# Kernel tuning notes

Measured on AMD Instinct MI355X. Metric: run time of the kernel, lower is better.

The kernel has to match this reference:

```python
import jax, jax.numpy as jnp
import numpy as np
from jax import lax

B, T, C = 32, 4096, 64
K, D, H, OUT = 256, 64, 512, 6

def _conv1d(x, w, b, stride):
    # x: [B, Cin, L], w: [Cout, Cin, k]
    y = lax.conv_general_dilated(x, w, (stride,), 'SAME',
                                 dimension_numbers=('NCH', 'OIH', 'NCH'))
    return y + b[None, :, None]

def _lstm_layer(x, wih, whh, b):
    # x: [B, T, in]; wih: [4H, in]; whh: [4H, H]
    Bb = x.shape[0]
    Hh = whh.shape[1]
    xg = jnp.einsum('bti,gi->btg', x, wih) + b          # [B, T, 4H] precomputed input gates
    def step(carry, g_t):
        h, c = carry
        gates = g_t + h @ whh.T
        i, f, g, o = jnp.split(gates, 4, axis=-1)        # torch gate order i,f,g,o
        i = jax.nn.sigmoid(i); f = jax.nn.sigmoid(f)
        g = jnp.tanh(g);       o = jax.nn.sigmoid(o)
        c = f * c + i * g
        h = o * jnp.tanh(c)
        return (h, c), h
    init = (jnp.zeros((Bb, Hh), x.dtype), jnp.zeros((Bb, Hh), x.dtype))
    _, hs = lax.scan(step, init, jnp.swapaxes(xg, 0, 1))
    return jnp.swapaxes(hs, 0, 1)                        # [B, T, H]

def setup_inputs() -> dict:
    key = jax.random.key(0)
    ks = jax.random.split(key, 12)
    s = 0.02
    return {
        'x':       jax.random.normal(ks[0], (B, T, C), jnp.float32),
        'conv_w1': jax.random.normal(ks[1], (64, 1, 4), jnp.float32) * s,
        'conv_b1': jnp.zeros((64,), jnp.float32),
        'conv_w2': jax.random.normal(ks[2], (64, 64, 4), jnp.float32) * s,
        'conv_b2': jnp.zeros((64,), jnp.float32),
        'conv_w3': jax.random.normal(ks[3], (64, 64, 3), jnp.float32) * s,
        'conv_b3': jnp.zeros((64,), jnp.float32),
        'codebook': jax.random.normal(ks[4], (K, D), jnp.float32),
        'wih0': jax.random.normal(ks[5], (4 * H, D), jnp.float32) * s,
        'whh0': jax.random.normal(ks[6], (4 * H, H), jnp.float32) * s,
        'bl0':  jnp.zeros((4 * H,), jnp.float32),
        'wih1': jax.random.normal(ks[7], (4 * H, H), jnp.float32) * s,
        'whh1': jax.random.normal(ks[8], (4 * H, H), jnp.float32) * s,
        'bl1':  jnp.zeros((4 * H,), jnp.float32),
        'w_out': jax.random.normal(ks[9], (OUT, H), jnp.float32) * s,
        'b_out': jnp.zeros((OUT,), jnp.float32),
    }

def reference(x, conv_w1, conv_b1, conv_w2, conv_b2, conv_w3, conv_b3,
              codebook, wih0, whh0, bl0, wih1, whh1, bl1, w_out, b_out):
    # ---- tokenizer (batched; replaces the per-sample python loop) ----
    sig = x.mean(axis=2)[:, None, :]                     # [B, 1, T] channel-mean 1D signal
    h1 = jax.nn.relu(_conv1d(sig, conv_w1, conv_b1, 2))   # [B, 64, T/2]
    h2 = jax.nn.relu(_conv1d(h1, conv_w2, conv_b2, 2))    # [B, 64, T/4]
    ze = _conv1d(h2, conv_w3, conv_b3, 1)                 # [B, D, T'] latents
    ze = jnp.swapaxes(ze, 1, 2)                           # [B, T', D]
    # nearest-code lookup: ||z - e||^2 argmin
    d = (jnp.sum(ze * ze, -1, keepdims=True)
         - 2.0 * ze @ codebook.T
         + jnp.sum(codebook * codebook, -1)[None, None, :])
    idx = jnp.argmin(d, axis=-1)                          # [B, T'] token indices
    # ---- codebook embedding gather ----
    z = codebook[idx]                                     # [B, T', D]
    # ---- 2-layer LSTM + per-step linear head ----
    h = _lstm_layer(z, wih0, whh0, bl0)
    h = _lstm_layer(h, wih1, whh1, bl1)
    preds = jnp.einsum('bth,oh->bto', h, w_out) + b_out   # [B, T', OUT]
    return preds
```

## Files before the change

### kernel.cpp

```cpp
#include <hip/hip_runtime.h>

constexpr int nB = 32, nT = 4096, nK = 256, nTP = 1024;

__device__ __forceinline__ float sigmoidf_(float x) { return 1.f / (1.f + expf(-x)); }

typedef unsigned int u32x4 __attribute__((ext_vector_type(4)));

__device__ __forceinline__ void store_u32_wt(unsigned* p, unsigned v) {
  asm volatile("global_store_dword %0, %1, off sc0 sc1" :: "v"(p), "v"(v) : "memory");
}
__device__ __forceinline__ void store_f32_wt(float* p, float v) {
  asm volatile("global_store_dword %0, %1, off sc0 sc1" :: "v"(p), "v"(v) : "memory");
}
__device__ __forceinline__ unsigned load_u32_wt(const unsigned* p) {
  unsigned v;
  asm volatile("global_load_dword %0, %1, off sc0 sc1\n\ts_waitcnt vmcnt(0)"
               : "=&v"(v) : "v"(p) : "memory");
  return v;
}

__device__ __forceinline__ float dpp_xor1(float x) {
  return __int_as_float(__builtin_amdgcn_update_dpp(0, __float_as_int(x), 0xB1, 0xF, 0xF, true));
}
__device__ __forceinline__ float dpp_xor2(float x) {
  return __int_as_float(__builtin_amdgcn_update_dpp(0, __float_as_int(x), 0x4E, 0xF, 0xF, true));
}
__device__ __forceinline__ float dpp_xor8(float x) {
  return __int_as_float(__builtin_amdgcn_update_dpp(0, __float_as_int(x), 0x128, 0xF, 0xF, true));
}
__device__ __forceinline__ float swz_xor4(float x) {
  return __int_as_float(__builtin_amdgcn_ds_swizzle(__float_as_int(x), 0x101F));
}
__device__ __forceinline__ float swz_xor16(float x) {
  return __int_as_float(__builtin_amdgcn_ds_swizzle(__float_as_int(x), 0x401F));
}


__global__ __launch_bounds__(256) void k_mean(const float* __restrict__ x, float* __restrict__ sig) {
  int row = blockIdx.x * 4 + (threadIdx.x >> 6);
  int lane = threadIdx.x & 63;
  float v = x[(size_t)row * 64 + lane];
  #pragma unroll
  for (int off = 32; off > 0; off >>= 1) v += __shfl_down(v, off, 64);
  if (lane == 0) sig[row] = v * (1.0f / 64.0f);
}

__global__ __launch_bounds__(256) void k_conv1(const float* __restrict__ sig,
    const float* __restrict__ w1, const float* __restrict__ b1, float* __restrict__ h1) {
  int idx = blockIdx.x * 256 + threadIdx.x;
  int o = idx & 2047;
  int co = (idx >> 11) & 63;
  int b = idx >> 17;
  const float* s = sig + (size_t)b * nT;
  float acc = b1[co];
  int base = 2 * o - 1;
  #pragma unroll
  for (int j = 0; j < 4; j++) {
    int p = base + j;
    float sv = (p >= 0 && p < nT) ? s[p] : 0.f;
    acc = fmaf(w1[co * 4 + j], sv, acc);
  }
  h1[idx] = fmaxf(acc, 0.f);
}

__global__ __launch_bounds__(256) void k_conv2(const float* __restrict__ h1,
    const float* __restrict__ w2, const float* __restrict__ b2, float* __restrict__ h2) {
  int blk = blockIdx.x;
  int otile = blk & 3, co = (blk >> 2) & 63, b = blk >> 8;
  int o = otile * 256 + threadIdx.x;
  __shared__ float w[256];
  w[threadIdx.x] = w2[co * 256 + threadIdx.x];
  __syncthreads();
  const float* hin = h1 + (size_t)b * 64 * 2048;
  float acc = b2[co];
  int base = 2 * o - 1;
  for (int ci = 0; ci < 64; ci++) {
    const float* r = hin + ci * 2048;
    const float* wc = w + ci * 4;
    #pragma unroll
    for (int j = 0; j < 4; j++) {
      int p = base + j;
      float v = (p >= 0 && p < 2048) ? r[p] : 0.f;
      acc = fmaf(wc[j], v, acc);
    }
  }
  h2[((size_t)b * 64 + co) * 1024 + o] = fmaxf(acc, 0.f);
}

__global__ __launch_bounds__(256) void k_conv3(const float* __restrict__ h2,
    const float* __restrict__ w3, const float* __restrict__ b3, float* __restrict__ ze) {
  int blk = blockIdx.x;
  int otile = blk & 3, co = (blk >> 2) & 63, b = blk >> 8;
  int o = otile * 256 + threadIdx.x;
  __shared__ float w[192];
  if (threadIdx.x < 192) w[threadIdx.x] = w3[co * 192 + threadIdx.x];
  __syncthreads();
  const float* hin = h2 + (size_t)b * 64 * 1024;
  float acc = b3[co];
  for (int ci = 0; ci < 64; ci++) {
    const float* r = hin + ci * 1024;
    const float* wc = w + ci * 3;
    #pragma unroll
    for (int j = 0; j < 3; j++) {
      int p = o - 1 + j;
      float v = (p >= 0 && p < 1024) ? r[p] : 0.f;
      acc = fmaf(wc[j], v, acc);
    }
  }
  ze[((size_t)b * 64 + co) * 1024 + o] = acc;
}

__global__ __launch_bounds__(256) void k_cbnorm(const float* __restrict__ cb, float* __restrict__ cbn) {
  int k = threadIdx.x;
  const float4* c4 = (const float4*)(cb + (size_t)k * 64);
  float acc = 0.f;
  #pragma unroll
  for (int q = 0; q < 16; q++) {
    float4 e = c4[q];
    acc = fmaf(e.x, e.x, fmaf(e.y, e.y, fmaf(e.z, e.z, fmaf(e.w, e.w, acc))));
  }
  cbn[k] = acc;
}

__global__ __launch_bounds__(256) void k_vq(const float* __restrict__ ze,
    const float* __restrict__ cb, const float* __restrict__ cbn, float* __restrict__ zq) {
  __shared__ float scb[nK * 64];
  for (int i = threadIdx.x; i < nK * 64; i += 256) scb[i] = cb[i];
  __syncthreads();
  int g = blockIdx.x * 256 + threadIdx.x;
  int b = g >> 10, o = g & 1023;
  const float* zb = ze + (size_t)b * 64 * 1024 + o;
  float z[64];
  #pragma unroll
  for (int d = 0; d < 64; d++) z[d] = zb[(size_t)d * 1024];
  float best = 3.4e38f; int bi = 0;
  for (int k = 0; k < nK; k++) {
    const float4* ck = (const float4*)(scb + k * 64);
    float dot = 0.f;
    #pragma unroll
    for (int q = 0; q < 16; q++) {
      float4 c4 = ck[q];
      dot = fmaf(c4.x, z[4 * q + 0], dot);
      dot = fmaf(c4.y, z[4 * q + 1], dot);
      dot = fmaf(c4.z, z[4 * q + 2], dot);
      dot = fmaf(c4.w, z[4 * q + 3], dot);
    }
    float s = cbn[k] - 2.f * dot;
    if (s < best) { best = s; bi = k; }
  }
  float4* zo4 = (float4*)(zq + (size_t)g * 64);
  const float4* cbest = (const float4*)(scb + bi * 64);
  #pragma unroll
  for (int q = 0; q < 16; q++) zo4[q] = cbest[q];
}

__global__ __launch_bounds__(256) void k_zqt(const float* __restrict__ zq, float* __restrict__ zqT) {
  int t = blockIdx.x;
  for (int o = threadIdx.x; o < 2048; o += 256) {
    int d = o >> 5, b = o & 31;
    zqT[(size_t)t * 2048 + o] = zq[((size_t)b * nTP + t) * 64 + d];
  }
}


__global__ __launch_bounds__(512, 2) void k_lstm(
    const float* __restrict__ zqT,
    const float* __restrict__ wih0, const float* __restrict__ whh0, const float* __restrict__ bl0,
    const float* __restrict__ wih1, const float* __restrict__ whh1, const float* __restrict__ bl1,
    const float* __restrict__ wout, const float* __restrict__ bout,
    float* __restrict__ st, float* __restrict__ out)
{
  __shared__ float wB [2][4][32][36];
  __shared__ float wAh[2][4][32][20];
  __shared__ float wAz[2][4][64];
  __shared__ float wHd[2][512];
  __shared__ float bHd[2];
  __shared__ float h0s[16384];

  float* h0T = st;
  float* h1T = st + 32768;
  unsigned* flags = (unsigned*)(st + 65536);
  unsigned* rel   = flags + 1024;

  const int blk = blockIdx.x;
  const int tid = threadIdx.x;
  const int dim = tid >> 8;
  const int bg  = (tid >> 5) & 7;
  const int c   = tid & 31;
  const int b0  = bg * 4;
  const int j   = 2 * blk + dim;

  for (int idx = tid; idx < 2 * 4 * 32 * 32; idx += 512) {
    int k = idx & 31, cc = (idx >> 5) & 31, gg = (idx >> 10) & 3, dd = idx >> 12;
    int row = gg * 512 + 2 * blk + dd;
    float v = (cc < 16) ? whh1[(size_t)row * 512 + cc * 32 + k]
                        : wih1[(size_t)row * 512 + (cc - 16) * 32 + k];
    wB[dd][gg][cc][k] = v;
  }
  for (int idx = tid; idx < 2 * 4 * 32 * 16; idx += 512) {
    int k = idx & 15, cc = (idx >> 4) & 31, gg = (idx >> 9) & 3, dd = idx >> 11;
    wAh[dd][gg][cc][k] = whh0[(size_t)(gg * 512 + 2 * blk + dd) * 512 + cc * 16 + k];
  }
  if (tid < 512) {
    int d = tid & 63, gg = (tid >> 6) & 3, dd = tid >> 8;
    wAz[dd][gg][d] = wih0[(size_t)(gg * 512 + 2 * blk + dd) * 64 + d];
  }
  if (blk < 96) {
    for (int idx = tid; idx < 1024; idx += 512) {
      int q = idx >> 9, i = idx & 511;
      int p = blk * 2 + q;
      wHd[q][i] = wout[(size_t)(p >> 5) * 512 + i];
      if (i == 0) bHd[q] = bout[p >> 5];
    }
  }
  float bA[4], bB4[4];
  #pragma unroll
  for (int g = 0; g < 4; g++) { bA[g] = bl0[g * 512 + j]; bB4[g] = bl1[g * 512 + j]; }
  float creg0 = 0.f, creg1 = 0.f;
  __syncthreads();

  const float* h0vL0 = h0s + ((c * 512 + b0) ^ ((c & 7) << 2));
  const int cp = c - 16;
  const float* h0vA = h0s + (((cp < 0 ? 0 : cp) * 1024 + b0) ^ (((2 * (cp < 0 ? 0 : cp)) & 7) << 2));
  const float* h0vB = h0s + (((cp < 0 ? 0 : cp) * 1024 + 512 + b0) ^ (((2 * (cp < 0 ? 0 : cp) + 1) & 7) << 2));

  for (int t = 0; t <= nTP + 1; t++) {
    if (t <= nTP) {
      const float* src = h0T + (t & 1) * 16384;
      #pragma unroll
      for (int q = 0; q < 8; q++) {
        int lin = (q * 512 + tid) * 4;
        float4 v = *(const float4*)(src + lin);
        int phys = lin ^ (((lin >> 9) & 7) << 2);
        *(float4*)&h0s[phys] = v;
      }
      __syncthreads();
    }

    if (t < nTP) {
      float acc[16];
      #pragma unroll
      for (int r = 0; r < 16; r++) acc[r] = 0.f;
      {
        #pragma unroll
        for (int s = 0; s < 4; s++) {
          float4 v0 = *(const float4*)(h0vL0 + (s * 4 + 0) * 32);
          float4 v1 = *(const float4*)(h0vL0 + (s * 4 + 1) * 32);
          float4 v2 = *(const float4*)(h0vL0 + (s * 4 + 2) * 32);
          float4 v3 = *(const float4*)(h0vL0 + (s * 4 + 3) * 32);
          #pragma unroll
          for (int g = 0; g < 4; g++) {
            float4 w = *(const float4*)&wAh[dim][g][c][s * 4];
            float* a = acc + g * 4;
            a[0]=fmaf(w.x,v0.x,a[0]); a[0]=fmaf(w.y,v1.x,a[0]); a[0]=fmaf(w.z,v2.x,a[0]); a[0]=fmaf(w.w,v3.x,a[0]);
            a[1]=fmaf(w.x,v0.y,a[1]); a[1]=fmaf(w.y,v1.y,a[1]); a[1]=fmaf(w.z,v2.y,a[1]); a[1]=fmaf(w.w,v3.y,a[1]);
            a[2]=fmaf(w.x,v0.z,a[2]); a[2]=fmaf(w.y,v1.z,a[2]); a[2]=fmaf(w.z,v2.z,a[2]); a[2]=fmaf(w.w,v3.z,a[2]);
            a[3]=fmaf(w.x,v0.w,a[3]); a[3]=fmaf(w.y,v1.w,a[3]); a[3]=fmaf(w.z,v2.w,a[3]); a[3]=fmaf(w.w,v3.w,a[3]);
          }
        }
      }
      {
        const float* zt = zqT + (size_t)t * 2048 + b0;
        float4 u0 = *(const float4*)(zt + (c * 2 + 0) * 32);
        float4 u1 = *(const float4*)(zt + (c * 2 + 1) * 32);
        #pragma unroll
        for (int g = 0; g < 4; g++) {
          float wx = wAz[dim][g][c * 2 + 0], wy = wAz[dim][g][c * 2 + 1];
          float* a = acc + g * 4;
          a[0]=fmaf(wx,u0.x,a[0]); a[0]=fmaf(wy,u1.x,a[0]);
          a[1]=fmaf(wx,u0.y,a[1]); a[1]=fmaf(wy,u1.y,a[1]);
          a[2]=fmaf(wx,u0.z,a[2]); a[2]=fmaf(wy,u1.z,a[2]);
          a[3]=fmaf(wx,u0.w,a[3]); a[3]=fmaf(wy,u1.w,a[3]);
        }
      }
      #pragma unroll
      for (int r = 0; r < 16; r++) acc[r] += dpp_xor1(acc[r]);
      #pragma unroll
      for (int r = 0; r < 16; r++) acc[r] += dpp_xor2(acc[r]);
      #pragma unroll
      for (int r = 0; r < 16; r++) acc[r] += swz_xor4(acc[r]);
      #pragma unroll
      for (int r = 0; r < 16; r++) acc[r] += dpp_xor8(acc[r]);
      #pragma unroll
      for (int r = 0; r < 16; r++) acc[r] += swz_xor16(acc[r]);
      if (c < 4) {
        int b = b0 + c;
        float gi = sigmoidf_(acc[0 * 4 + c] + bA[0]);
        float gf = sigmoidf_(acc[1 * 4 + c] + bA[1]);
        float gg = tanhf    (acc[2 * 4 + c] + bA[2]);
        float go = sigmoidf_(acc[3 * 4 + c] + bA[3]);
        float cn = fmaf(gf, creg0, gi * gg);
        creg0 = cn;
        store_f32_wt(h0T + ((t + 1) & 1) * 16384 + j * 32 + b, go * tanhf(cn));
      }
    }

    if (t >= 1 && t <= nTP) {
      const float* h1p = h1T + ((t - 1) & 1) * 16384;
      float4 vbuf[32];
      if (c < 16) {
        const float* vg = h1p + c * 32 * 32 + b0;
        #pragma unroll
        for (int k = 0; k < 32; k++) vbuf[k] = *(const float4*)(vg + k * 32);
      } else {
        #pragma unroll
        for (int k = 0; k < 16; k++) vbuf[k] = *(const float4*)(h0vA + k * 32);
        #pragma unroll
        for (int k = 0; k < 16; k++) vbuf[16 + k] = *(const float4*)(h0vB + k * 32);
      }
      float acc[16];
      #pragma unroll
      for (int r = 0; r < 16; r++) acc[r] = 0.f;
      #pragma unroll
      for (int s = 0; s < 8; s++) {
        float4 v0 = vbuf[s * 4 + 0];
        float4 v1 = vbuf[s * 4 + 1];
        float4 v2 = vbuf[s * 4 + 2];
        float4 v3 = vbuf[s * 4 + 3];
        #pragma unroll
        for (int g = 0; g < 4; g++) {
          float4 w = *(const float4*)&wB[dim][g][c][s * 4];
          float* a = acc + g * 4;
          a[0]=fmaf(w.x,v0.x,a[0]); a[0]=fmaf(w.y,v1.x,a[0]); a[0]=fmaf(w.z,v2.x,a[0]); a[0]=fmaf(w.w,v3.x,a[0]);
          a[1]=fmaf(w.x,v0.y,a[1]); a[1]=fmaf(w.y,v1.y,a[1]); a[1]=fmaf(w.z,v2.y,a[1]); a[1]=fmaf(w.w,v3.y,a[1]);
          a[2]=fmaf(w.x,v0.z,a[2]); a[2]=fmaf(w.y,v1.z,a[2]); a[2]=fmaf(w.z,v2.z,a[2]); a[2]=fmaf(w.w,v3.z,a[2]);
          a[3]=fmaf(w.x,v0.w,a[3]); a[3]=fmaf(w.y,v1.w,a[3]); a[3]=fmaf(w.z,v2.w,a[3]); a[3]=fmaf(w.w,v3.w,a[3]);
        }
      }
      #pragma unroll
      for (int r = 0; r < 16; r++) acc[r] += dpp_xor1(acc[r]);
      #pragma unroll
      for (int r = 0; r < 16; r++) acc[r] += dpp_xor2(acc[r]);
      #pragma unroll
      for (int r = 0; r < 16; r++) acc[r] += swz_xor4(acc[r]);
      #pragma unroll
      for (int r = 0; r < 16; r++) acc[r] += dpp_xor8(acc[r]);
      #pragma unroll
      for (int r = 0; r < 16; r++) acc[r] += swz_xor16(acc[r]);
      if (c < 4) {
        int b = b0 + c;
        float gi = sigmoidf_(acc[0 * 4 + c] + bB4[0]);
        float gf = sigmoidf_(acc[1 * 4 + c] + bB4[1]);
        float gg = tanhf    (acc[2 * 4 + c] + bB4[2]);
        float go = sigmoidf_(acc[3 * 4 + c] + bB4[3]);
        float cn = fmaf(gf, creg1, gi * gg);
        creg1 = cn;
        store_f32_wt(h1T + (t & 1) * 16384 + j * 32 + b, go * tanhf(cn));
      }
    }

    asm volatile("s_waitcnt vmcnt(0)" ::: "memory");
    __syncthreads();

    if (t <= nTP && tid == 0) store_u32_wt(flags + blk, (unsigned)(t + 1));

    if (t >= 2 && blk < 96 && tid >= 64 && tid < 80) {
      int q = (tid >> 3) & 1, l = tid & 7;
      int p = blk * 2 + q;
      int b = p & 31;
      const float* h1s = h1T + ((t - 1) & 1) * 16384;
      float a = 0.f;
      #pragma unroll 8
      for (int m = 0; m < 64; m++) {
        int i = l * 64 + m;
        a = fmaf(wHd[q][i], h1s[i * 32 + b], a);
      }
      a += __shfl_down(a, 4, 8);
      a += __shfl_down(a, 2, 8);
      a += __shfl_down(a, 1, 8);
      if (l == 0) out[((size_t)b * nTP + (t - 2)) * 6 + (p >> 5)] = a + bHd[q];
    }

    if (t <= nTP) {
      unsigned tgt = (unsigned)(t + 1);
      if (blk == 0) {
        if (tid < 64) {
          const u32x4* fp = (const u32x4*)flags + tid;
          for (;;) {
            u32x4 f;
            asm volatile("global_load_dwordx4 %0, %1, off sc0 sc1\n\ts_waitcnt vmcnt(0)"
                         : "=&v"(f) : "v"(fp) : "memory");
            bool ok = (f.x >= tgt) && (f.y >= tgt) && (f.z >= tgt) && (f.w >= tgt);
            if (__all(ok)) break;
            __builtin_amdgcn_s_sleep(1);
          }
          unsigned* rp = rel + tid * 64;
          #pragma unroll
          for (int q = 0; q < 4; q++) store_u32_wt(rp + q * 16, tgt);
          __builtin_amdgcn_fence(__ATOMIC_ACQUIRE, "agent");
        }
      } else {
        if (tid == 0) {
          const unsigned* rp = rel + blk * 16;
          while (load_u32_wt(rp) < tgt) __builtin_amdgcn_s_sleep(1);
        }
        if (tid < 64) __builtin_amdgcn_fence(__ATOMIC_ACQUIRE, "agent");
      }
      __syncthreads();
    }
  }
}


extern "C" void kernel_launch(void* const* d_in, const int* in_sizes, int n_in,
                              void* d_out, int out_size, void* d_ws, size_t ws_size,
                              hipStream_t stream) {
  (void)in_sizes; (void)n_in; (void)out_size; (void)ws_size;
  const float* x    = (const float*)d_in[0];
  const float* w1   = (const float*)d_in[1];
  const float* b1   = (const float*)d_in[2];
  const float* w2   = (const float*)d_in[3];
  const float* b2   = (const float*)d_in[4];
  const float* w3   = (const float*)d_in[5];
  const float* b3   = (const float*)d_in[6];
  const float* cb   = (const float*)d_in[7];
  const float* wih0 = (const float*)d_in[8];
  const float* whh0 = (const float*)d_in[9];
  const float* bl0  = (const float*)d_in[10];
  const float* wih1 = (const float*)d_in[11];
  const float* whh1 = (const float*)d_in[12];
  const float* bl1  = (const float*)d_in[13];
  const float* wout = (const float*)d_in[14];
  const float* bout = (const float*)d_in[15];
  float* out = (float*)d_out;

  float* ws  = (float*)d_ws;
  float* sig = ws;
  float* h1c = sig + 131072;
  float* h2c = h1c + 4194304;
  float* ze  = h2c + 2097152;
  float* zq  = ze  + 2097152;
  float* cbn = zq  + 2097152;
  float* stp = ws;
  float* zqT = h1c;

  k_mean <<<32768, 256, 0, stream>>>(x, sig);
  k_conv1<<<16384, 256, 0, stream>>>(sig, w1, b1, h1c);
  hipMemsetAsync(stp, 0, (65536 + 1024 + 4096) * sizeof(float), stream);
  k_conv2<<<8192, 256, 0, stream>>>(h1c, w2, b2, h2c);
  k_conv3<<<8192, 256, 0, stream>>>(h2c, w3, b3, ze);
  k_cbnorm<<<1, 256, 0, stream>>>(cb, cbn);
  k_vq   <<<128, 256, 0, stream>>>(ze, cb, cbn, zq);
  k_zqt  <<<1024, 256, 0, stream>>>(zq, zqT);

  void* kargs[] = { (void*)&zqT, (void*)&wih0, (void*)&whh0, (void*)&bl0,
                    (void*)&wih1, (void*)&whh1, (void*)&bl1,
                    (void*)&wout, (void*)&bout, (void*)&stp, (void*)&out };
  hipLaunchCooperativeKernel((void*)k_lstm, dim3(256), dim3(512), kargs, 0, stream);
}
```

Before: 15.24 ms.

## Split LSTM grid barrier into per-layer barriers with triple-buffered states

Replaces the single grid-wide barrier per timestep with separate flag/release barriers for layer 0 and layer 1. The hidden-state buffers become three-deep. Layer-0 results are published before layer-1 computes, so the layer-0 barrier can complete while layer-1 work and the output head run. The aim is to hide barrier latency on the critical recurrence path, at the cost of two barrier rounds per step and more spin-polling traffic.

```diff
diff --git a/kernel.cpp b/kernel.cpp
--- a/kernel.cpp
+++ b/kernel.cpp
@@ -178,9 +178,11 @@
   __shared__ float h0s[16384];
 
   float* h0T = st;
-  float* h1T = st + 32768;
-  unsigned* flags = (unsigned*)(st + 65536);
-  unsigned* rel   = flags + 1024;
+  float* h1T = st + 49152;
+  unsigned* flags0 = (unsigned*)(st + 98304);
+  unsigned* flags1 = flags0 + 1024;
+  unsigned* rel0   = flags1 + 1024;
+  unsigned* rel1   = rel0 + 4096;
 
   const int blk = blockIdx.x;
   const int tid = threadIdx.x;
@@ -225,8 +227,24 @@
   const float* h0vB = h0s + (((cp < 0 ? 0 : cp) * 1024 + 512 + b0) ^ (((2 * (cp < 0 ? 0 : cp) + 1) & 7) << 2));
 
   for (int t = 0; t <= nTP + 1; t++) {
+    const int p  = t % 3;
+    const int pw = (p + 1 == 3) ? 0 : p + 1;
+    const int pm = (p + 2 >= 3) ? p - 1 : p + 2;
+
+    if (t >= 1 && t <= nTP) {
+      if (tid == 0) {
+        unsigned tg0 = (unsigned)t, tg1 = (unsigned)(t - 1);
+        const unsigned* rp0 = rel0 + blk * 16;
+        const unsigned* rp1 = rel1 + blk * 16;
+        while (load_u32_wt(rp0) < tg0) __builtin_amdgcn_s_sleep(1);
+        while (load_u32_wt(rp1) < tg1) __builtin_amdgcn_s_sleep(1);
+      }
+      if (tid < 64) __builtin_amdgcn_fence(__ATOMIC_ACQUIRE, "agent");
+      __syncthreads();
+    }
+
     if (t <= nTP) {
-      const float* src = h0T + (t & 1) * 16384;
+      const float* src = h0T + p * 16384;
       #pragma unroll
       for (int q = 0; q < 8; q++) {
         int lin = (q * 512 + tid) * 4;
@@ -291,12 +309,42 @@
         float go = sigmoidf_(acc[3 * 4 + c] + bA[3]);
         float cn = fmaf(gf, creg0, gi * gg);
         creg0 = cn;
-        store_f32_wt(h0T + ((t + 1) & 1) * 16384 + j * 32 + b, go * tanhf(cn));
-      }
+        store_f32_wt(h0T + pw * 16384 + j * 32 + b, go * tanhf(cn));
+      }
+    }
+
+    asm volatile("s_waitcnt vmcnt(0)" ::: "memory");
+    __syncthreads();
+    if (t < nTP && tid == 0) store_u32_wt(flags0 + blk, (unsigned)(t + 1));
+
+    if (t < nTP && blk == 0 && tid < 64) {
+      unsigned tgt = (unsigned)(t + 1);
+      const u32x4* fp = (const u32x4*)flags0 + tid;
+      for (;;) {
+        u32x4 f;
+        asm volatile("global_load_dwordx4 %0, %1, off sc0 sc1\n\ts_waitcnt vmcnt(0)"
+                     : "=&v"(f) : "v"(fp) : "memory");
+        bool ok = (f.x >= tgt) && (f.y >= tgt) && (f.z >= tgt) && (f.w >= tgt);
+        if (__all(ok)) break;
+        __builtin_amdgcn_s_sleep(1);
+      }
+      unsigned* rp = rel0 + tid * 64;
+      #pragma unroll
+      for (int q = 0; q < 4; q++) store_u32_wt(rp + q * 16, tgt);
+    }
+
+    if (t >= 1) {
+      if (tid == 0) {
+        unsigned tg1 = (unsigned)t;
+        const unsigned* rp1 = rel1 + blk * 16;
+        while (load_u32_wt(rp1) < tg1) __builtin_amdgcn_s_sleep(1);
+      }
+      if (tid < 64) __builtin_amdgcn_fence(__ATOMIC_ACQUIRE, "agent");
+      __syncthreads();
     }
 
     if (t >= 1 && t <= nTP) {
-      const float* h1p = h1T + ((t - 1) & 1) * 16384;
+      const float* h1p = h1T + pm * 16384;
       float4 vbuf[32];
       if (c < 16) {
         const float* vg = h1p + c * 32 * 32 + b0;
@@ -345,20 +393,15 @@
         float go = sigmoidf_(acc[3 * 4 + c] + bB4[3]);
         float cn = fmaf(gf, creg1, gi * gg);
         creg1 = cn;
-        store_f32_wt(h1T + (t & 1) * 16384 + j * 32 + b, go * tanhf(cn));
-      }
-    }
-
-    asm volatile("s_waitcnt vmcnt(0)" ::: "memory");
-    __syncthreads();
-
-    if (t <= nTP && tid == 0) store_u32_wt(flags + blk, (unsigned)(t + 1));
+        store_f32_wt(h1T + p * 16384 + j * 32 + b, go * tanhf(cn));
+      }
+    }
 
     if (t >= 2 && blk < 96 && tid >= 64 && tid < 80) {
       int q = (tid >> 3) & 1, l = tid & 7;
-      int p = blk * 2 + q;
-      int b = p & 31;
-      const float* h1s = h1T + ((t - 1) & 1) * 16384;
+      int pp = blk * 2 + q;
+      int b = pp & 31;
+      const float* h1s = h1T + pm * 16384;
       float a = 0.f;
       #pragma unroll 8
       for (int m = 0; m < 64; m++) {
@@ -368,35 +411,27 @@
       a += __shfl_down(a, 4, 8);
       a += __shfl_down(a, 2, 8);
       a += __shfl_down(a, 1, 8);
-      if (l == 0) out[((size_t)b * nTP + (t - 2)) * 6 + (p >> 5)] = a + bHd[q];
-    }
-
-    if (t <= nTP) {
+      if (l == 0) out[((size_t)b * nTP + (t - 2)) * 6 + (pp >> 5)] = a + bHd[q];
+    }
+
+    asm volatile("s_waitcnt vmcnt(0)" ::: "memory");
+    __syncthreads();
+    if (t <= nTP && tid == 0) store_u32_wt(flags1 + blk, (unsigned)(t + 1));
+
+    if (t <= nTP && blk == 0 && tid < 64) {
       unsigned tgt = (unsigned)(t + 1);
-      if (blk == 0) {
-        if (tid < 64) {
-          const u32x4* fp = (const u32x4*)flags + tid;
-          for (;;) {
-            u32x4 f;
-            asm volatile("global_load_dwordx4 %0, %1, off sc0 sc1\n\ts_waitcnt vmcnt(0)"
-                         : "=&v"(f) : "v"(fp) : "memory");
-            bool ok = (f.x >= tgt) && (f.y >= tgt) && (f.z >= tgt) && (f.w >= tgt);
-            if (__all(ok)) break;
-            __builtin_amdgcn_s_sleep(1);
-          }
-          unsigned* rp = rel + tid * 64;
-          #pragma unroll
-          for (int q = 0; q < 4; q++) store_u32_wt(rp + q * 16, tgt);
-          __builtin_amdgcn_fence(__ATOMIC_ACQUIRE, "agent");
-        }
-      } else {
-        if (tid == 0) {
-          const unsigned* rp = rel + blk * 16;
-          while (load_u32_wt(rp) < tgt) __builtin_amdgcn_s_sleep(1);
-        }
-        if (tid < 64) __builtin_amdgcn_fence(__ATOMIC_ACQUIRE, "agent");
-      }
-      __syncthreads();
+      const u32x4* fp = (const u32x4*)flags1 + tid;
+      for (;;) {
+        u32x4 f;
+        asm volatile("global_load_dwordx4 %0, %1, off sc0 sc1\n\ts_waitcnt vmcnt(0)"
+                     : "=&v"(f) : "v"(fp) : "memory");
+        bool ok = (f.x >= tgt) && (f.y >= tgt) && (f.z >= tgt) && (f.w >= tgt);
+        if (__all(ok)) break;
+        __builtin_amdgcn_s_sleep(1);
+      }
+      unsigned* rp = rel1 + tid * 64;
+      #pragma unroll
+      for (int q = 0; q < 4; q++) store_u32_wt(rp + q * 16, tgt);
     }
   }
 }
@@ -436,7 +471,7 @@
 
   k_mean <<<32768, 256, 0, stream>>>(x, sig);
   k_conv1<<<16384, 256, 0, stream>>>(sig, w1, b1, h1c);
-  hipMemsetAsync(stp, 0, (65536 + 1024 + 4096) * sizeof(float), stream);
+  hipMemsetAsync(stp, 0, (98304 + 2048 + 8192) * sizeof(float), stream);
   k_conv2<<<8192, 256, 0, stream>>>(h1c, w2, b2, h2c);
   k_conv3<<<8192, 256, 0, stream>>>(h2c, w3, b3, ze);
   k_cbnorm<<<1, 256, 0, stream>>>(cb, cbn);
```

Measured after the change: 17.42 ms. 14.4% more time.

## Replace acquire fences with sc0 sc1 cache-bypassing loads for cross-block state

Applied to the files above, without the earlier changes.

The per-step agent-scope acquire fences after the grid barrier are removed. They invalidate caches on every step. To keep cross-block visibility, the reads of shared hidden-state buffers (h0T, h1T and the head's h1 reads) now use inline-asm global loads with sc0 sc1 bits, all issued before a single vmcnt wait. This relies on those cache bits alone to observe other blocks' writes, which is a memory-ordering risk if any read still goes through a normal cached path.

```diff
diff --git a/kernel.cpp b/kernel.cpp
--- a/kernel.cpp
+++ b/kernel.cpp
@@ -5,6 +5,7 @@
 __device__ __forceinline__ float sigmoidf_(float x) { return 1.f / (1.f + expf(-x)); }
 
 typedef unsigned int u32x4 __attribute__((ext_vector_type(4)));
+typedef float f32x4v __attribute__((ext_vector_type(4)));
 
 __device__ __forceinline__ void store_u32_wt(unsigned* p, unsigned v) {
   asm volatile("global_store_dword %0, %1, off sc0 sc1" :: "v"(p), "v"(v) : "memory");
@@ -16,6 +17,16 @@
   unsigned v;
   asm volatile("global_load_dword %0, %1, off sc0 sc1\n\ts_waitcnt vmcnt(0)"
                : "=&v"(v) : "v"(p) : "memory");
+  return v;
+}
+__device__ __forceinline__ f32x4v load_f32x4_wt_nw(const float* p) {
+  f32x4v v;
+  asm volatile("global_load_dwordx4 %0, %1, off sc0 sc1" : "=&v"(v) : "v"(p) : "memory");
+  return v;
+}
+__device__ __forceinline__ float load_f32_wt_nw(const float* p) {
+  float v;
+  asm volatile("global_load_dword %0, %1, off sc0 sc1" : "=&v"(v) : "v"(p) : "memory");
   return v;
 }
 
@@ -227,12 +238,16 @@
   for (int t = 0; t <= nTP + 1; t++) {
     if (t <= nTP) {
       const float* src = h0T + (t & 1) * 16384;
+      f32x4v sv[8];
+      #pragma unroll
+      for (int q = 0; q < 8; q++) sv[q] = load_f32x4_wt_nw(src + (q * 512 + tid) * 4);
+      asm volatile("s_waitcnt vmcnt(0)" ::: "memory");
+      __builtin_amdgcn_sched_barrier(0);
       #pragma unroll
       for (int q = 0; q < 8; q++) {
         int lin = (q * 512 + tid) * 4;
-        float4 v = *(const float4*)(src + lin);
         int phys = lin ^ (((lin >> 9) & 7) << 2);
-        *(float4*)&h0s[phys] = v;
+        *(f32x4v*)&h0s[phys] = sv[q];
       }
       __syncthreads();
     }
@@ -297,26 +312,28 @@
 
     if (t >= 1 && t <= nTP) {
       const float* h1p = h1T + ((t - 1) & 1) * 16384;
-      float4 vbuf[32];
+      f32x4v vbuf[32];
       if (c < 16) {
         const float* vg = h1p + c * 32 * 32 + b0;
         #pragma unroll
-        for (int k = 0; k < 32; k++) vbuf[k] = *(const float4*)(vg + k * 32);
+        for (int k = 0; k < 32; k++) vbuf[k] = load_f32x4_wt_nw(vg + k * 32);
       } else {
         #pragma unroll
-        for (int k = 0; k < 16; k++) vbuf[k] = *(const float4*)(h0vA + k * 32);
-        #pragma unroll
-        for (int k = 0; k < 16; k++) vbuf[16 + k] = *(const float4*)(h0vB + k * 32);
-      }
+        for (int k = 0; k < 16; k++) vbuf[k] = *(const f32x4v*)(h0vA + k * 32);
+        #pragma unroll
+        for (int k = 0; k < 16; k++) vbuf[16 + k] = *(const f32x4v*)(h0vB + k * 32);
+      }
+      asm volatile("s_waitcnt vmcnt(0)" ::: "memory");
+      __builtin_amdgcn_sched_barrier(0);
       float acc[16];
       #pragma unroll
       for (int r = 0; r < 16; r++) acc[r] = 0.f;
       #pragma unroll
       for (int s = 0; s < 8; s++) {
-        float4 v0 = vbuf[s * 4 + 0];
-        float4 v1 = vbuf[s * 4 + 1];
-        float4 v2 = vbuf[s * 4 + 2];
-        float4 v3 = vbuf[s * 4 + 3];
+        f32x4v v0 = vbuf[s * 4 + 0];
+        f32x4v v1 = vbuf[s * 4 + 1];
+        f32x4v v2 = vbuf[s * 4 + 2];
+        f32x4v v3 = vbuf[s * 4 + 3];
         #pragma unroll
         for (int g = 0; g < 4; g++) {
           float4 w = *(const float4*)&wB[dim][g][c][s * 4];
@@ -359,12 +376,14 @@
       int p = blk * 2 + q;
       int b = p & 31;
       const float* h1s = h1T + ((t - 1) & 1) * 16384;
+      float hv[64];
+      #pragma unroll
+      for (int m = 0; m < 64; m++) hv[m] = load_f32_wt_nw(h1s + (l * 64 + m) * 32 + b);
+      asm volatile("s_waitcnt vmcnt(0)" ::: "memory");
+      __builtin_amdgcn_sched_barrier(0);
       float a = 0.f;
-      #pragma unroll 8
-      for (int m = 0; m < 64; m++) {
-        int i = l * 64 + m;
-        a = fmaf(wHd[q][i], h1s[i * 32 + b], a);
-      }
+      #pragma unroll
+      for (int m = 0; m < 64; m++) a = fmaf(wHd[q][l * 64 + m], hv[m], a);
       a += __shfl_down(a, 4, 8);
       a += __shfl_down(a, 2, 8);
       a += __shfl_down(a, 1, 8);
@@ -387,14 +406,12 @@
           unsigned* rp = rel + tid * 64;
           #pragma unroll
           for (int q = 0; q < 4; q++) store_u32_wt(rp + q * 16, tgt);
-          __builtin_amdgcn_fence(__ATOMIC_ACQUIRE, "agent");
         }
       } else {
         if (tid == 0) {
           const unsigned* rp = rel + blk * 16;
           while (load_u32_wt(rp) < tgt) __builtin_amdgcn_s_sleep(1);
         }
-        if (tid < 64) __builtin_amdgcn_fence(__ATOMIC_ACQUIRE, "agent");
       }
       __syncthreads();
     }
```

Result: faster. 14.27 ms (-6.4%).
